# Performance work log

Measured on AMD Instinct MI355X. Metric: run time of the kernel, lower is better.

Reference implementation:

```python
import jax, jax.numpy as jnp
import numpy as np

BATCH = 4096
IN_DIM = 512
OUT_DIM = 512
GRID_SIZE = 5
K = 3


def _extended_grid():
    # Original: grid = linspace(-1, 1, grid_size+1), spacing h = 2/grid_size.
    # The de Boor-Cox recursion in the source indexes up to grid[grid_size+2k],
    # so we extend the uniform grid to the right with the same spacing.
    h = 2.0 / GRID_SIZE
    return (-1.0 + h * jnp.arange(GRID_SIZE + 2 * K + 1)).astype(jnp.float32)


def bspline_basis(x, grid, k):
    """Vectorized de Boor-Cox recursion.
    x: [..., ] floats; returns basis [..., grid_size + k].
    Identical math to the recursive b_spline_basis in the source, but computed
    bottom-up over all knot intervals at once (no redundant recomputation).
    """
    xe = x[..., None]  # [..., 1]
    # degree-0: indicator of half-open knot intervals, [..., n_knots-1]
    B = ((grid[:-1] <= xe) & (xe < grid[1:])).astype(x.dtype)
    for d in range(1, k + 1):
        n = grid.shape[0] - d - 1
        gi, gid = grid[:n], grid[d:d + n]          # grid[i], grid[i+d]
        gi1, gid1 = grid[1:n + 1], grid[d + 1:d + n + 1]  # grid[i+1], grid[i+d+1]
        # uniform grid -> denominators are d*h, never zero
        B = (xe - gi) / (gid - gi) * B[..., :n] + (gid1 - xe) / (gid1 - gi1) * B[..., 1:n + 1]
    return B  # [..., grid_size + k]


def setup_inputs() -> dict:
    key = jax.random.key(0)
    k1, k2 = jax.random.split(key)
    x = jax.random.uniform(k1, (BATCH, IN_DIM), jnp.float32) * 2.0 - 1.0  # in [-1, 1)
    spline_coeff = jax.random.normal(k2, (IN_DIM, OUT_DIM, GRID_SIZE + K), jnp.float32)
    spline_scaling = jnp.ones((IN_DIM, OUT_DIM), jnp.float32)
    return {"x": x, "spline_coeff": spline_coeff, "spline_scaling": spline_scaling}


def reference(x, spline_coeff, spline_scaling):
    grid = _extended_grid()
    basis = bspline_basis(x, grid, K)  # [B, in_dim, grid_size+k]
    # out[b, j] = sum_i scaling[i,j] * sum_g basis[b,i,g] * coeff[i,j,g]
    return jnp.einsum('big,ijg,ij->bj', basis, spline_coeff, spline_scaling)
```

## Files before the change

### kernel.cpp

```cpp
#include <hip/hip_runtime.h>
#include <hip/hip_bf16.h>
#include <stdint.h>


#define BATCH   4096
#define IN_DIM  512
#define OUT_DIM 512
#define KDIM    (IN_DIM * 8)
#define NKT     (KDIM / 64)

typedef short short8 __attribute__((ext_vector_type(8)));
typedef float f32x4  __attribute__((ext_vector_type(4)));

#define W_VM6_LG0  0x076
#define W_VM8_LG0  0x078
#define W_VM10_LG0 0x07A

__device__ __forceinline__ unsigned int f2bf(float f) {
  union { float f; unsigned int u; } v; v.f = f;
  unsigned int r = v.u + 0x7FFFu + ((v.u >> 16) & 1u);
  return r >> 16;
}

__device__ __forceinline__ short8 basis_pack8(float xv) {
  float t = __builtin_fmaf(xv, 2.5f, 2.5f);
  int m = (int)t;
  m = m > 4 ? 4 : m;
  float u  = t - (float)m;
  float u2 = u * u, u3 = u2 * u, om = 1.0f - u;
  float om2 = om * om;
  float w0 = om2 * om * (1.0f / 6.0f);
  float w1 = __builtin_fmaf(u3, 0.5f, __builtin_fmaf(u2, -1.0f, 2.0f / 3.0f));
  float s  = (u2 - u3) + u;
  float w2 = __builtin_fmaf(s, 0.5f, 1.0f / 6.0f);
  float w3 = u3 * (1.0f / 6.0f);
  unsigned d0 = __builtin_amdgcn_perm(__float_as_uint(w1), __float_as_uint(w0), 0x07060302u);
  unsigned d1 = __builtin_amdgcn_perm(__float_as_uint(w3), __float_as_uint(w2), 0x07060302u);
  uint64_t wp = ((uint64_t)d1 << 32) | d0;
  int sh = m * 16 - 48;
  uint64_t lo = (sh >= 0) ? (wp << sh) : (wp >> (-sh));
  unsigned hi = (sh > 0) ? (unsigned)(wp >> (64 - sh)) : 0u;
  union { unsigned d[4]; short8 s8; } r;
  r.d[0] = (unsigned)lo; r.d[1] = (unsigned)(lo >> 32); r.d[2] = hi; r.d[3] = 0u;
  return r.s8;
}

__device__ __forceinline__ void async_load16(const void* g, void* l) {
  __builtin_amdgcn_global_load_lds(
      (__attribute__((address_space(1))) void*)(uintptr_t)g,
      (__attribute__((address_space(3))) void*)(unsigned int)(uintptr_t)l,
      16, 0, 0);
}
__device__ __forceinline__ void async_load4(const void* g, void* l) {
  __builtin_amdgcn_global_load_lds(
      (__attribute__((address_space(1))) void*)(uintptr_t)g,
      (__attribute__((address_space(3))) void*)(unsigned int)(uintptr_t)l,
      4, 0, 0);
}

__global__ void kan_prep(const float* __restrict__ coeff,
                         const float* __restrict__ scaling,
                         unsigned short* __restrict__ Wt) {
  int idx = blockIdx.x * 256 + threadIdx.x;
  int i = idx >> 9, j = idx & 511;
  float s = scaling[idx];
  const float4* cp = reinterpret_cast<const float4*>(coeff) + (size_t)idx * 2;
  float4 c0 = cp[0], c1 = cp[1];
  short8 h;
  h[0] = (short)f2bf(c0.x * s); h[1] = (short)f2bf(c0.y * s);
  h[2] = (short)f2bf(c0.z * s); h[3] = (short)f2bf(c0.w * s);
  h[4] = (short)f2bf(c1.x * s); h[5] = (short)f2bf(c1.y * s);
  h[6] = (short)f2bf(c1.z * s); h[7] = (short)f2bf(c1.w * s);
  *reinterpret_cast<short8*>(Wt + (size_t)j * KDIM + i * 8) = h;
}

__global__ __launch_bounds__(256, 2)
void kan_gemm_p(const float* __restrict__ x,
                const unsigned short* __restrict__ Wt,
                float* __restrict__ out) {
  __shared__ unsigned short As[4][64 * 64];
  __shared__ unsigned short Bs[4][64 * 64];
  __shared__ float          Xs[4][512];

  const int tid  = threadIdx.x;
  const int lane = tid & 63;
  const int wid  = tid >> 6;
  const int wm = wid >> 1, wn = wid & 1;
  const int ln = lane & 15, quad = lane >> 4;

  const int b    = blockIdx.x;
  const int row0 = (b & 63) * 64;
  const int col0 = (b >> 6) * 64;

  f32x4 acc[2][2] = {};

  const int lr = lane >> 3;
  const int cg = (lane & 7) ^ lr;
  const unsigned short* bBase0 = Wt + (size_t)(col0 + wid * 16 + lr) * KDIM + cg * 8;
  const unsigned short* bBase1 = bBase0 + (size_t)8 * KDIM;

  const int f0 = wid * 128 + lane;
  const int f1 = f0 + 64;
  const float* xBase0 = x + (size_t)(row0 + (f0 >> 3)) * IN_DIM + (f0 & 7);
  const float* xBase1 = x + (size_t)(row0 + (f1 >> 3)) * IN_DIM + (f1 & 7);

  const int rn  = lane;
  const int sw0 = ((wid * 2)     ^ (rn & 7)) * 8;
  const int sw1 = ((wid * 2 + 1) ^ (rn & 7)) * 8;

  int aoff[2][2], boff[2][2];
#pragma unroll
  for (int kk = 0; kk < 2; ++kk) {
#pragma unroll
    for (int mt = 0; mt < 2; ++mt) {
      const int r = wm * 32 + mt * 16 + ln;
      aoff[kk][mt] = r * 64 + (((kk * 4 + quad) ^ (r & 7)) * 8);
      const int c = wn * 32 + mt * 16 + ln;
      boff[kk][mt] = c * 64 + (((kk * 4 + quad) ^ (c & 7)) * 8);
    }
  }

  auto issueB = [&](int kt, int st) {
    const int k0 = kt * 64;
    async_load16(bBase0 + k0, &Bs[st][(wid * 16) * 64]);
    async_load16(bBase1 + k0, &Bs[st][(wid * 16 + 8) * 64]);
  };
  auto issueX = [&](int kt, int st) {
    async_load4(xBase0 + kt * 8, &Xs[st][wid * 128]);
    async_load4(xBase1 + kt * 8, &Xs[st][wid * 128 + 64]);
  };
  auto computeA = [&](float2 xv, int st) {
    short8 h0 = basis_pack8(xv.x);
    short8 h1 = basis_pack8(xv.y);
    *reinterpret_cast<short8*>(&As[st][rn * 64 + sw0]) = h0;
    *reinterpret_cast<short8*>(&As[st][rn * 64 + sw1]) = h1;
  };
  auto compute = [&](int st) {
#pragma unroll
    for (int kk = 0; kk < 2; ++kk) {
      short8 af[2], bfr[2];
#pragma unroll
      for (int mt = 0; mt < 2; ++mt)
        af[mt] = *reinterpret_cast<const short8*>(&As[st][aoff[kk][mt]]);
#pragma unroll
      for (int nt = 0; nt < 2; ++nt)
        bfr[nt] = *reinterpret_cast<const short8*>(&Bs[st][boff[kk][nt]]);
#pragma unroll
      for (int mt = 0; mt < 2; ++mt)
#pragma unroll
        for (int nt = 0; nt < 2; ++nt)
          acc[mt][nt] = __builtin_amdgcn_mfma_f32_16x16x32_bf16(af[mt], bfr[nt], acc[mt][nt], 0, 0, 0);
    }
  };

  issueX(0, 0); issueX(1, 1);
  issueX(2, 2); issueB(0, 0);
  __builtin_amdgcn_s_waitcnt(W_VM6_LG0);
  __builtin_amdgcn_s_barrier();
  { float2 xv = *reinterpret_cast<const float2*>(&Xs[0][rn * 8 + wid * 2]); computeA(xv, 0); }
  issueX(3, 3); issueB(1, 1);
  __builtin_amdgcn_s_waitcnt(W_VM8_LG0);
  __builtin_amdgcn_s_barrier();
  { float2 xv = *reinterpret_cast<const float2*>(&Xs[1][rn * 8 + wid * 2]); computeA(xv, 1); }
  issueX(4, 0); issueB(2, 2);
  __builtin_amdgcn_s_waitcnt(W_VM10_LG0);
  __builtin_amdgcn_s_barrier();
  { float2 xv = *reinterpret_cast<const float2*>(&Xs[2][rn * 8 + wid * 2]); computeA(xv, 2); }

  for (int g = 0; g < 16; ++g) {
#pragma unroll
    for (int s = 0; s < 4; ++s) {
      const int kt = g * 4 + s;
      __builtin_amdgcn_s_waitcnt(W_VM6_LG0);
      __builtin_amdgcn_s_barrier();
      float2 xv = *reinterpret_cast<const float2*>(&Xs[(s + 3) & 3][rn * 8 + wid * 2]);
      const int kx = (kt + 5 < NKT) ? kt + 5 : NKT - 1;
      const int kb = (kt + 3 < NKT) ? kt + 3 : NKT - 1;
      issueX(kx, (s + 1) & 3);
      issueB(kb, (s + 3) & 3);
      compute(s);
      computeA(xv, (s + 3) & 3);
    }
  }

#pragma unroll
  for (int mt = 0; mt < 2; ++mt)
#pragma unroll
    for (int nt = 0; nt < 2; ++nt) {
      const int col = col0 + wn * 32 + nt * 16 + ln;
#pragma unroll
      for (int r = 0; r < 4; ++r) {
        const int row = row0 + wm * 32 + mt * 16 + quad * 4 + r;
        out[(size_t)row * OUT_DIM + col] = acc[mt][nt][r];
      }
    }
}

__global__ __launch_bounds__(256, 2)
void kan_gemm_fb(const float* __restrict__ x, const float* __restrict__ coeff,
                 const float* __restrict__ scaling, float* __restrict__ out) {
  __shared__ unsigned short As[64 * 64];
  __shared__ unsigned short Bs[64 * 64];

  const int tid  = threadIdx.x;
  const int lane = tid & 63;
  const int wid  = tid >> 6;
  const int wm = wid >> 1, wn = wid & 1;
  const int ln = lane & 15, quad = lane >> 4;
  const int row0 = blockIdx.y * 64;
  const int col0 = blockIdx.x * 64;

  f32x4 acc[2][2] = {};

  for (int kt = 0; kt < KDIM / 64; ++kt) {
#pragma unroll
    for (int pp = 0; pp < 2; ++pp) {
      const int p  = tid + pp * 256;
      const int rn = p & 63;
      const int il = p >> 6;
      const int sw = ((il ^ (rn & 7)) * 8);
      short8 ha = basis_pack8(x[(size_t)(row0 + rn) * IN_DIM + kt * 8 + il]);
      *reinterpret_cast<short8*>(&As[rn * 64 + sw]) = ha;
      const float* cbase = coeff + (size_t)(kt * 8 + il) * 4096 + (size_t)(col0 + rn) * 8;
      float4 c0 = reinterpret_cast<const float4*>(cbase)[0];
      float4 c1 = reinterpret_cast<const float4*>(cbase)[1];
      float s = scaling[(size_t)(kt * 8 + il) * OUT_DIM + col0 + rn];
      short8 hb;
      hb[0] = (short)f2bf(c0.x * s); hb[1] = (short)f2bf(c0.y * s);
      hb[2] = (short)f2bf(c0.z * s); hb[3] = (short)f2bf(c0.w * s);
      hb[4] = (short)f2bf(c1.x * s); hb[5] = (short)f2bf(c1.y * s);
      hb[6] = (short)f2bf(c1.z * s); hb[7] = (short)f2bf(c1.w * s);
      *reinterpret_cast<short8*>(&Bs[rn * 64 + sw]) = hb;
    }
    __syncthreads();
#pragma unroll
    for (int kk = 0; kk < 2; ++kk) {
      short8 af[2], bfr[2];
#pragma unroll
      for (int mt = 0; mt < 2; ++mt) {
        const int r  = wm * 32 + mt * 16 + ln;
        const int pc = (kk * 4 + quad) ^ (r & 7);
        af[mt] = *reinterpret_cast<const short8*>(&As[r * 64 + pc * 8]);
      }
#pragma unroll
      for (int nt = 0; nt < 2; ++nt) {
        const int c  = wn * 32 + nt * 16 + ln;
        const int pc = (kk * 4 + quad) ^ (c & 7);
        bfr[nt] = *reinterpret_cast<const short8*>(&Bs[c * 64 + pc * 8]);
      }
#pragma unroll
      for (int mt = 0; mt < 2; ++mt)
#pragma unroll
        for (int nt = 0; nt < 2; ++nt)
          acc[mt][nt] = __builtin_amdgcn_mfma_f32_16x16x32_bf16(af[mt], bfr[nt], acc[mt][nt], 0, 0, 0);
    }
    __syncthreads();
  }
#pragma unroll
  for (int mt = 0; mt < 2; ++mt)
#pragma unroll
    for (int nt = 0; nt < 2; ++nt) {
      const int col = col0 + wn * 32 + nt * 16 + ln;
#pragma unroll
      for (int r = 0; r < 4; ++r) {
        const int row = row0 + wm * 32 + mt * 16 + quad * 4 + r;
        out[(size_t)row * OUT_DIM + col] = acc[mt][nt][r];
      }
    }
}

extern "C" void kernel_launch(void* const* d_in, const int* in_sizes, int n_in,
                              void* d_out, int out_size, void* d_ws, size_t ws_size,
                              hipStream_t stream) {
  const float* x       = (const float*)d_in[0];
  const float* coeff   = (const float*)d_in[1];
  const float* scaling = (const float*)d_in[2];
  float* out = (float*)d_out;

  const size_t needW = (size_t)OUT_DIM * KDIM * 2;

  if (ws_size >= needW) {
    unsigned short* Wt = (unsigned short*)d_ws;
    kan_prep<<<(IN_DIM * OUT_DIM) / 256, 256, 0, stream>>>(coeff, scaling, Wt);
    kan_gemm_p<<<(BATCH / 64) * (OUT_DIM / 64), 256, 0, stream>>>(x, Wt, out);
  } else {
    kan_gemm_fb<<<dim3(OUT_DIM / 64, BATCH / 64), 256, 0, stream>>>(x, coeff, scaling, out);
  }
}
```

Measured before the change: 107.7 us.

## Compute B-spline basis in registers as MFMA A-operand, enlarge tile to 128x64

The GEMM kernel no longer stages x and the bf16 basis through LDS. Each wave loads its x values straight into registers with a two-deep prefetch and builds the MFMA A fragments in registers, so only W tiles go through LDS. The block tile grows to 128 rows by 64 columns, with each wave owning 32 rows across all 64 columns. This removes the LDS writes and reads for A and their barrier dependency, and reuses each B fragment across two MFMAs. In exchange each wave recomputes basis values per k-step, uses more accumulator registers, and the grid has half as many blocks.

Result: slower. 120.7 us (+12.0%).

```diff
diff --git a/kernel.cpp b/kernel.cpp
--- a/kernel.cpp
+++ b/kernel.cpp
@@ -12,9 +12,7 @@
 typedef short short8 __attribute__((ext_vector_type(8)));
 typedef float f32x4  __attribute__((ext_vector_type(4)));
 
-#define W_VM6_LG0  0x076
-#define W_VM8_LG0  0x078
-#define W_VM10_LG0 0x07A
+#define W_VM12_LG0 0x07C
 
 __device__ __forceinline__ unsigned int f2bf(float f) {
   union { float f; unsigned int u; } v; v.f = f;
@@ -51,12 +49,6 @@
       (__attribute__((address_space(3))) void*)(unsigned int)(uintptr_t)l,
       16, 0, 0);
 }
-__device__ __forceinline__ void async_load4(const void* g, void* l) {
-  __builtin_amdgcn_global_load_lds(
-      (__attribute__((address_space(1))) void*)(uintptr_t)g,
-      (__attribute__((address_space(3))) void*)(unsigned int)(uintptr_t)l,
-      4, 0, 0);
-}
 
 __global__ void kan_prep(const float* __restrict__ coeff,
                          const float* __restrict__ scaling,
@@ -75,122 +67,97 @@
 }
 
 __global__ __launch_bounds__(256, 2)
-void kan_gemm_p(const float* __restrict__ x,
+void kan_gemm_r(const float* __restrict__ x,
                 const unsigned short* __restrict__ Wt,
                 float* __restrict__ out) {
-  __shared__ unsigned short As[4][64 * 64];
   __shared__ unsigned short Bs[4][64 * 64];
-  __shared__ float          Xs[4][512];
 
   const int tid  = threadIdx.x;
   const int lane = tid & 63;
   const int wid  = tid >> 6;
-  const int wm = wid >> 1, wn = wid & 1;
   const int ln = lane & 15, quad = lane >> 4;
 
   const int b    = blockIdx.x;
-  const int row0 = (b & 63) * 64;
-  const int col0 = (b >> 6) * 64;
-
-  f32x4 acc[2][2] = {};
+  const int row0 = (b & 31) * 128;
+  const int col0 = (b >> 5) * 64;
+
+  f32x4 acc[2][4] = {};
 
   const int lr = lane >> 3;
   const int cg = (lane & 7) ^ lr;
-  const unsigned short* bBase0 = Wt + (size_t)(col0 + wid * 16 + lr) * KDIM + cg * 8;
-  const unsigned short* bBase1 = bBase0 + (size_t)8 * KDIM;
-
-  const int f0 = wid * 128 + lane;
-  const int f1 = f0 + 64;
-  const float* xBase0 = x + (size_t)(row0 + (f0 >> 3)) * IN_DIM + (f0 & 7);
-  const float* xBase1 = x + (size_t)(row0 + (f1 >> 3)) * IN_DIM + (f1 & 7);
-
-  const int rn  = lane;
-  const int sw0 = ((wid * 2)     ^ (rn & 7)) * 8;
-  const int sw1 = ((wid * 2 + 1) ^ (rn & 7)) * 8;
-
-  int aoff[2][2], boff[2][2];
-#pragma unroll
-  for (int kk = 0; kk < 2; ++kk) {
-#pragma unroll
-    for (int mt = 0; mt < 2; ++mt) {
-      const int r = wm * 32 + mt * 16 + ln;
-      aoff[kk][mt] = r * 64 + (((kk * 4 + quad) ^ (r & 7)) * 8);
-      const int c = wn * 32 + mt * 16 + ln;
-      boff[kk][mt] = c * 64 + (((kk * 4 + quad) ^ (c & 7)) * 8);
-    }
-  }
+  const unsigned short* bP0 = Wt + (size_t)(col0 + wid * 16 + lr) * KDIM + cg * 8;
+  const unsigned short* bP1 = bP0 + (size_t)8 * KDIM;
+
+  const float* xP0 = x + (size_t)(row0 + wid * 32 + ln) * IN_DIM + quad;
+  const float* xP1 = xP0 + (size_t)16 * IN_DIM;
+
+  int boff[2][4];
+#pragma unroll
+  for (int kk = 0; kk < 2; ++kk)
+#pragma unroll
+    for (int nt = 0; nt < 4; ++nt) {
+      const int c = nt * 16 + ln;
+      boff[kk][nt] = c * 64 + (((kk * 4 + quad) ^ (c & 7)) * 8);
+    }
 
   auto issueB = [&](int kt, int st) {
     const int k0 = kt * 64;
-    async_load16(bBase0 + k0, &Bs[st][(wid * 16) * 64]);
-    async_load16(bBase1 + k0, &Bs[st][(wid * 16 + 8) * 64]);
+    async_load16(bP0 + k0, &Bs[st][(wid * 16) * 64]);
+    async_load16(bP1 + k0, &Bs[st][(wid * 16 + 8) * 64]);
   };
-  auto issueX = [&](int kt, int st) {
-    async_load4(xBase0 + kt * 8, &Xs[st][wid * 128]);
-    async_load4(xBase1 + kt * 8, &Xs[st][wid * 128 + 64]);
+
+  float xa[2][2][2];
+  auto loadx = [&](int t, int buf) {
+#pragma unroll
+    for (int kk = 0; kk < 2; ++kk) {
+      xa[buf][0][kk] = xP0[t * 8 + kk * 4];
+      xa[buf][1][kk] = xP1[t * 8 + kk * 4];
+    }
   };
-  auto computeA = [&](float2 xv, int st) {
-    short8 h0 = basis_pack8(xv.x);
-    short8 h1 = basis_pack8(xv.y);
-    *reinterpret_cast<short8*>(&As[st][rn * 64 + sw0]) = h0;
-    *reinterpret_cast<short8*>(&As[st][rn * 64 + sw1]) = h1;
-  };
-  auto compute = [&](int st) {
-#pragma unroll
-    for (int kk = 0; kk < 2; ++kk) {
-      short8 af[2], bfr[2];
-#pragma unroll
-      for (int mt = 0; mt < 2; ++mt)
-        af[mt] = *reinterpret_cast<const short8*>(&As[st][aoff[kk][mt]]);
-#pragma unroll
-      for (int nt = 0; nt < 2; ++nt)
-        bfr[nt] = *reinterpret_cast<const short8*>(&Bs[st][boff[kk][nt]]);
-#pragma unroll
-      for (int mt = 0; mt < 2; ++mt)
-#pragma unroll
-        for (int nt = 0; nt < 2; ++nt)
-          acc[mt][nt] = __builtin_amdgcn_mfma_f32_16x16x32_bf16(af[mt], bfr[nt], acc[mt][nt], 0, 0, 0);
-    }
-  };
-
-  issueX(0, 0); issueX(1, 1);
-  issueX(2, 2); issueB(0, 0);
-  __builtin_amdgcn_s_waitcnt(W_VM6_LG0);
-  __builtin_amdgcn_s_barrier();
-  { float2 xv = *reinterpret_cast<const float2*>(&Xs[0][rn * 8 + wid * 2]); computeA(xv, 0); }
-  issueX(3, 3); issueB(1, 1);
-  __builtin_amdgcn_s_waitcnt(W_VM8_LG0);
-  __builtin_amdgcn_s_barrier();
-  { float2 xv = *reinterpret_cast<const float2*>(&Xs[1][rn * 8 + wid * 2]); computeA(xv, 1); }
-  issueX(4, 0); issueB(2, 2);
-  __builtin_amdgcn_s_waitcnt(W_VM10_LG0);
-  __builtin_amdgcn_s_barrier();
-  { float2 xv = *reinterpret_cast<const float2*>(&Xs[2][rn * 8 + wid * 2]); computeA(xv, 2); }
+
+  issueB(0, 0);
+  issueB(1, 1);
+  loadx(0, 0);
+  issueB(2, 2);
+  loadx(1, 1);
 
   for (int g = 0; g < 16; ++g) {
 #pragma unroll
     for (int s = 0; s < 4; ++s) {
       const int kt = g * 4 + s;
-      __builtin_amdgcn_s_waitcnt(W_VM6_LG0);
+      __builtin_amdgcn_s_waitcnt(W_VM12_LG0);
       __builtin_amdgcn_s_barrier();
-      float2 xv = *reinterpret_cast<const float2*>(&Xs[(s + 3) & 3][rn * 8 + wid * 2]);
-      const int kx = (kt + 5 < NKT) ? kt + 5 : NKT - 1;
+      float cur[2][2];
+#pragma unroll
+      for (int mt = 0; mt < 2; ++mt)
+#pragma unroll
+        for (int kk = 0; kk < 2; ++kk) cur[mt][kk] = xa[s & 1][mt][kk];
       const int kb = (kt + 3 < NKT) ? kt + 3 : NKT - 1;
-      issueX(kx, (s + 1) & 3);
+      const int kx = (kt + 2 < NKT) ? kt + 2 : NKT - 1;
       issueB(kb, (s + 3) & 3);
-      compute(s);
-      computeA(xv, (s + 3) & 3);
+      loadx(kx, s & 1);
+#pragma unroll
+      for (int kk = 0; kk < 2; ++kk) {
+        short8 af0 = basis_pack8(cur[0][kk]);
+        short8 af1 = basis_pack8(cur[1][kk]);
+#pragma unroll
+        for (int nt = 0; nt < 4; ++nt) {
+          short8 bfr = *reinterpret_cast<const short8*>(&Bs[s][boff[kk][nt]]);
+          acc[0][nt] = __builtin_amdgcn_mfma_f32_16x16x32_bf16(af0, bfr, acc[0][nt], 0, 0, 0);
+          acc[1][nt] = __builtin_amdgcn_mfma_f32_16x16x32_bf16(af1, bfr, acc[1][nt], 0, 0, 0);
+        }
+      }
     }
   }
 
 #pragma unroll
   for (int mt = 0; mt < 2; ++mt)
 #pragma unroll
-    for (int nt = 0; nt < 2; ++nt) {
-      const int col = col0 + wn * 32 + nt * 16 + ln;
+    for (int nt = 0; nt < 4; ++nt) {
+      const int col = col0 + nt * 16 + ln;
 #pragma unroll
       for (int r = 0; r < 4; ++r) {
-        const int row = row0 + wm * 32 + mt * 16 + quad * 4 + r;
+        const int row = row0 + wid * 32 + mt * 16 + quad * 4 + r;
         out[(size_t)row * OUT_DIM + col] = acc[mt][nt][r];
       }
     }
@@ -282,7 +249,7 @@
   if (ws_size >= needW) {
     unsigned short* Wt = (unsigned short*)d_ws;
     kan_prep<<<(IN_DIM * OUT_DIM) / 256, 256, 0, stream>>>(coeff, scaling, Wt);
-    kan_gemm_p<<<(BATCH / 64) * (OUT_DIM / 64), 256, 0, stream>>>(x, Wt, out);
+    kan_gemm_r<<<(BATCH / 128) * (OUT_DIM / 64), 256, 0, stream>>>(x, Wt, out);
   } else {
     kan_gemm_fb<<<dim3(OUT_DIM / 64, BATCH / 64), 256, 0, stream>>>(x, coeff, scaling, out);
   }
```
